# Kernel optimization log

Hardware: AMD Instinct MI355X
Metric: run time of the kernel (lower is better)

## Reference

```python
import jax, jax.numpy as jnp
import numpy as np

D_MODEL = 1024
D_FF = 4096          # shared expert hidden
NUM_M = 2
E_ROUTER = 8 * NUM_M - 1   # 15 router experts
D_FF_R = D_FF // NUM_M     # 2048 router expert hidden
TOP_K = NUM_M * 2 - 1      # 3
B, T = 2, 2048


def setup_inputs() -> dict:
    key = jax.random.key(0)
    ks = jax.random.split(key, 12)
    s = lambda fan_in: 1.0 / np.sqrt(fan_in)
    x = jax.random.normal(ks[0], (B, T, D_MODEL), dtype=jnp.float32)
    # shared experts stacked [S=1, ...]
    sW1 = jax.random.uniform(ks[1], (1, D_MODEL, D_FF), jnp.float32, -s(D_MODEL), s(D_MODEL))
    sb1 = jax.random.uniform(ks[2], (1, D_FF), jnp.float32, -s(D_MODEL), s(D_MODEL))
    sW2 = jax.random.uniform(ks[3], (1, D_FF, D_MODEL), jnp.float32, -s(D_FF), s(D_FF))
    sb2 = jax.random.uniform(ks[4], (1, D_MODEL), jnp.float32, -s(D_FF), s(D_FF))
    # router experts stacked [E, ...]
    rW1 = jax.random.uniform(ks[5], (E_ROUTER, D_MODEL, D_FF_R), jnp.float32, -s(D_MODEL), s(D_MODEL))
    rb1 = jax.random.uniform(ks[6], (E_ROUTER, D_FF_R), jnp.float32, -s(D_MODEL), s(D_MODEL))
    rW2 = jax.random.uniform(ks[7], (E_ROUTER, D_FF_R, D_MODEL), jnp.float32, -s(D_FF_R), s(D_FF_R))
    rb2 = jax.random.uniform(ks[8], (E_ROUTER, D_MODEL), jnp.float32, -s(D_FF_R), s(D_FF_R))
    # gating linear d_model -> E
    gW = jax.random.uniform(ks[9], (D_MODEL, E_ROUTER), jnp.float32, -s(D_MODEL), s(D_MODEL))
    gb = jax.random.uniform(ks[10], (E_ROUTER,), jnp.float32, -s(D_MODEL), s(D_MODEL))
    return {"x": x, "sW1": sW1, "sb1": sb1, "sW2": sW2, "sb2": sb2,
            "rW1": rW1, "rb1": rb1, "rW2": rW2, "rb2": rb2, "gW": gW, "gb": gb}


def _expert_stack(x, W1, b1, W2, b2):
    # x: [b,t,d]; W1: [e,d,f] -> out [e,b,t,d]
    h = jax.nn.gelu(jnp.einsum('btd,edf->ebtf', x, W1) + b1[:, None, None, :],
                    approximate=False)
    return jnp.einsum('ebtf,efd->ebtd', h, W2) + b2[:, None, None, :]


def reference(x, sW1, sb1, sW2, sb2, rW1, rb1, rW2, rb2, gW, gb):
    # shared experts (sum over S)
    shared_enc = _expert_stack(x, sW1, sb1, sW2, sb2).sum(0)  # [b,t,d]
    # gating: softmax then keep top-k values (no renormalization)
    weights = jax.nn.softmax(x @ gW + gb, axis=-1)            # [b,t,E]
    topv, topi = jax.lax.top_k(weights, TOP_K)                # [b,t,K]
    gated = (jax.nn.one_hot(topi, E_ROUTER, dtype=weights.dtype)
             * topv[..., None]).sum(axis=-2)                  # [b,t,E]
    # dense per-expert compute masked by sparse gates (faithful to source)
    router_out = _expert_stack(x, rW1, rb1, rW2, rb2)         # [E,b,t,d]
    router_enc = jnp.einsum('ebtd,bte->btd', router_out, gated)
    return shared_enc + router_enc + x
```

## Files before the change

kernel.cpp:

```cpp
#include <hip/hip_runtime.h>
#include <hip/hip_bf16.h>
#include <cstdint>
#include <cstddef>

#define TOKENS 4096
#define DM     1024
#define DFF    4096
#define NE     15
#define DFR    2048
#define NEX    17
#define MAXT   176

typedef float f32x4 __attribute__((ext_vector_type(4)));
typedef int   i32x4 __attribute__((ext_vector_type(4)));

__device__ __forceinline__ void mfma_16x16x32_bf16(f32x4& d, i32x4 a, i32x4 b){
  asm("v_mfma_f32_16x16x32_bf16 %0, %1, %2, %0" : "+v"(d) : "v"(a), "v"(b));
}

__device__ __forceinline__ void gload16(const void* g, void* l){
  __builtin_amdgcn_global_load_lds(
      (const __attribute__((address_space(1))) uint32_t*)g,
      (__attribute__((address_space(3))) uint32_t*)l, 16, 0, 0);
}

__device__ __forceinline__ unsigned short f2bf(float f){
  unsigned u = __float_as_uint(f);
  u += 0x7FFFu + ((u >> 16) & 1u);
  return (unsigned short)(u >> 16);
}

__device__ __forceinline__ float gelu_exact(float v){
  return 0.5f * v * (1.0f + erff(v * 0.70710678118654752440f));
}


__global__ void cast_x_kernel(const float* __restrict__ x, ushort* __restrict__ xb, int n4){
  int i = blockIdx.x*256 + threadIdx.x;
  if (i >= n4) return;
  float4 v = reinterpret_cast<const float4*>(x)[i];
  ushort4 o; o.x=f2bf(v.x); o.y=f2bf(v.y); o.z=f2bf(v.z); o.w=f2bf(v.w);
  reinterpret_cast<ushort4*>(xb)[i] = o;
}

__global__ void tcast_kernel(const float* __restrict__ src, ushort* __restrict__ dst, int R, int C){
  __shared__ float tile[32][33];
  const size_t bo = (size_t)blockIdx.z * R * C;
  const int c0 = blockIdx.x*32, r0 = blockIdx.y*32;
  const int tx = threadIdx.x, ty = threadIdx.y;
  #pragma unroll
  for (int i=0;i<4;i++){
    int r = ty + i*8;
    tile[r][tx] = src[bo + (size_t)(r0+r)*C + c0 + tx];
  }
  __syncthreads();
  #pragma unroll
  for (int i=0;i<4;i++){
    int r = ty + i*8;
    dst[bo + (size_t)(c0+r)*R + r0 + tx] = f2bf(tile[tx][r]);
  }
}


__global__ void gate_kernel(const float* __restrict__ x, const float* __restrict__ gW,
                            const float* __restrict__ gb,
                            int* __restrict__ tokexp, float* __restrict__ tokp){
  const int wave = threadIdx.x >> 6, lane = threadIdx.x & 63;
  const int token = blockIdx.x*4 + wave;
  const float* xr = x + (size_t)token * DM;
  float a[NE];
  #pragma unroll
  for (int e=0;e<NE;e++) a[e] = 0.f;
  const int d0 = lane * 16;
  float xv[16];
  #pragma unroll
  for (int j=0;j<4;j++){
    float4 v = reinterpret_cast<const float4*>(xr + d0)[j];
    xv[j*4+0]=v.x; xv[j*4+1]=v.y; xv[j*4+2]=v.z; xv[j*4+3]=v.w;
  }
  for (int j=0;j<16;j++){
    const float* gr = gW + (size_t)(d0 + j) * NE;
    #pragma unroll
    for (int e=0;e<NE;e++) a[e] += xv[j]*gr[e];
  }
  #pragma unroll
  for (int e=0;e<NE;e++){
    for (int off=32; off; off>>=1) a[e] += __shfl_xor(a[e], off, 64);
  }
  if (lane == 0){
    float l[NE], p[NE];
    float m = -1e30f;
    for (int e=0;e<NE;e++){ l[e] = a[e] + gb[e]; m = fmaxf(m, l[e]); }
    float s = 0.f;
    for (int e=0;e<NE;e++){ p[e] = expf(l[e]-m); s += p[e]; }
    float inv = 1.f/s;
    unsigned used = 0;
    for (int k=0;k<3;k++){
      int best = -1; float bv = -1e30f;
      for (int e=0;e<NE;e++) if (!((used>>e)&1u) && l[e] > bv){ bv = l[e]; best = e; }
      used |= 1u<<best;
      tokexp[token*3 + k] = best;
      tokp[token*3 + k]   = p[best]*inv;
    }
  }
}


__global__ void assign_kernel(const int* __restrict__ tokexp, const float* __restrict__ tokp,
                              int* __restrict__ counts, int* __restrict__ bases,
                              int* __restrict__ tokidx, float* __restrict__ gatev,
                              int* __restrict__ tokslot,
                              int* __restrict__ tile_e, int* __restrict__ tile_by,
                              int* __restrict__ ntiles){
  __shared__ int lh[256][NE];
  const int tid = threadIdx.x;
  const int t0 = tid * 16;

  int le[48];
  #pragma unroll
  for (int e=0;e<NE;e++) lh[tid][e] = 0;
  #pragma unroll
  for (int j=0;j<48;j++){
    int e = tokexp[t0*3 + j];
    le[j] = e;
    lh[tid][e]++;
  }
  __syncthreads();
  if (tid < NE){
    int run = 0;
    for (int i=0;i<256;i++){
      int v = lh[i][tid];
      lh[i][tid] = run;
      run += v;
    }
    counts[tid] = run;
  }
  __syncthreads();
  if (tid == 0){
    int b = 0;
    int t = 0;
    for (int e=0;e<NE;e++){
      int c = counts[e];
      bases[e] = b; b += ((c+127)>>7)<<7;
      int nb = (c+127)>>7;
      for (int j=0;j<nb;j++){ tile_e[t]=e; tile_by[t]=j; t++; }
    }
    bases[NE] = b; bases[NE+1] = b + TOKENS;
    for (int e=NE;e<NEX;e++){
      for (int j=0;j<32;j++){ tile_e[t]=e; tile_by[t]=j; t++; }
    }
    ntiles[0] = t;
  }
  __syncthreads();
  #pragma unroll
  for (int j=0;j<48;j++){
    const int t = t0 + (j/3), k = j - (j/3)*3;
    const int e = le[j];
    const int slot = lh[tid][e]++;
    const int idx = e*TOKENS + slot;
    tokidx[idx] = t;
    gatev[idx]  = tokp[t*3 + k];
    tokslot[t*3 + k] = idx;
  }
}


__global__ __launch_bounds__(256,3) void gemm1_kernel(
    const ushort* __restrict__ xb, const ushort* __restrict__ rW1T,
    const ushort* __restrict__ sW1T, const float* __restrict__ rb1,
    const float* __restrict__ sb1, const int* __restrict__ counts,
    const int* __restrict__ bases, const int* __restrict__ tokidx,
    const int* __restrict__ tile_e, const int* __restrict__ tile_by,
    const int* __restrict__ ntiles, ushort* __restrict__ h)
{
  const int ty = blockIdx.y;
  if (ty >= ntiles[0]) return;
  const int e = tile_e[ty], by = tile_by[ty], bx = blockIdx.x;
  const int cnt = (e < NE) ? counts[e] : TOKENS;

  __shared__ __align__(16) ushort lA[128*64];
  __shared__ __align__(16) ushort lB[128*64];

  const int tid = threadIdx.x, wave = tid >> 6, lane = tid & 63;
  const int wr = wave >> 1, wc = wave & 1;

  const ushort* Bp = (e < NE) ? (rW1T + ((size_t)e*DFR + (size_t)bx*128)*DM)
                              : (sW1T + ((size_t)(e-NE)*DFR + (size_t)bx*128)*DM);

  const ushort* srcA[4];
  const ushort* srcB[4];
  unsigned ldso[4];
  #pragma unroll
  for (int i=0;i<4;i++){
    const int rt = i*32 + wave*8 + (lane>>3);
    const int gr = by*128 + rt;
    const int tok = (e < NE) ? tokidx[e*TOKENS + (gr < cnt ? gr : cnt-1)] : gr;
    srcA[i] = xb + (size_t)tok*DM + (lane&7)*8;
    srcB[i] = Bp + (size_t)rt*DM + (lane&7)*8;
    ldso[i] = (unsigned)(i*4096 + wave*1024 + lane*16);
  }

  f32x4 zv = {0.f,0.f,0.f,0.f};
  f32x4 acc[4][4];
  #pragma unroll
  for (int m=0;m<4;m++){
    #pragma unroll
    for (int n=0;n<4;n++){ acc[m][n] = zv; }
  }

  for (int k0=0; k0<DM; k0+=64){
    __syncthreads();
    #pragma unroll
    for (int i=0;i<4;i++){ gload16(srcA[i]+k0, (char*)lA + ldso[i]); }
    #pragma unroll
    for (int i=0;i<4;i++){ gload16(srcB[i]+k0, (char*)lB + ldso[i]); }
    __syncthreads();
    #pragma unroll
    for (int kk=0; kk<2; kk++){
      i32x4 af[4], bfr[4];
      #pragma unroll
      for (int m=0;m<4;m++){
        af[m] = *(const i32x4*)((const char*)lA + ((wr*64 + m*16 + (lane&15))*128 + kk*64 + (lane>>4)*16));
      }
      #pragma unroll
      for (int n=0;n<4;n++){
        bfr[n] = *(const i32x4*)((const char*)lB + ((wc*64 + n*16 + (lane&15))*128 + kk*64 + (lane>>4)*16));
      }
      #pragma unroll
      for (int m=0;m<4;m++){
        #pragma unroll
        for (int n=0;n<4;n++){ mfma_16x16x32_bf16(acc[m][n], af[m], bfr[n]); }
      }
    }
  }

  const int hb = bases[e];
  const float* b1p = (e < NE) ? (rb1 + e*DFR + bx*128) : (sb1 + (e-NE)*DFR + bx*128);
  #pragma unroll
  for (int m=0;m<4;m++){
    #pragma unroll
    for (int n=0;n<4;n++){
      const int c = wc*64 + n*16 + (lane & 15);
      const float bias = b1p[c];
      #pragma unroll
      for (int i=0;i<4;i++){
        const int r = wr*64 + m*16 + (lane>>4)*4 + i;
        float v = acc[m][n][i] + bias;
        h[(size_t)(hb + by*128 + r)*DFR + (size_t)bx*128 + c] = f2bf(gelu_exact(v));
      }
    }
  }
}


__global__ __launch_bounds__(256,3) void gemm2_kernel(
    const ushort* __restrict__ h, const ushort* __restrict__ rW2T,
    const ushort* __restrict__ sW2T, const float* __restrict__ rb2,
    const float* __restrict__ sb2, const int* __restrict__ counts,
    const int* __restrict__ bases,
    const int* __restrict__ tile_e, const int* __restrict__ tile_by,
    const int* __restrict__ ntiles, ushort* __restrict__ rout)
{
  const int ty = blockIdx.y;
  if (ty >= ntiles[0]) return;
  const int e = tile_e[ty], by = tile_by[ty], bx = blockIdx.x;

  __shared__ __align__(16) ushort lA[128*64];
  __shared__ __align__(16) ushort lB[128*64];

  const int tid = threadIdx.x, wave = tid >> 6, lane = tid & 63;
  const int wr = wave >> 1, wc = wave & 1;

  const int hb = bases[e];
  const ushort* Ab = h + (size_t)(hb + by*128)*DFR;
  const ushort* Bp; size_t ldb;
  if (e < NE){ Bp = rW2T + ((size_t)e*DM + (size_t)bx*128)*DFR; ldb = DFR; }
  else       { Bp = sW2T + (size_t)(bx*128)*DFF + (size_t)(e-NE)*DFR; ldb = DFF; }

  const ushort* srcA[4];
  const ushort* srcB[4];
  unsigned ldso[4];
  #pragma unroll
  for (int i=0;i<4;i++){
    const int rt = i*32 + wave*8 + (lane>>3);
    srcA[i] = Ab + (size_t)rt*DFR + (lane&7)*8;
    srcB[i] = Bp + (size_t)rt*ldb + (lane&7)*8;
    ldso[i] = (unsigned)(i*4096 + wave*1024 + lane*16);
  }

  f32x4 zv = {0.f,0.f,0.f,0.f};
  f32x4 acc[4][4];
  #pragma unroll
  for (int m=0;m<4;m++){
    #pragma unroll
    for (int n=0;n<4;n++){ acc[m][n] = zv; }
  }

  for (int k0=0; k0<DFR; k0+=64){
    __syncthreads();
    #pragma unroll
    for (int i=0;i<4;i++){ gload16(srcA[i]+k0, (char*)lA + ldso[i]); }
    #pragma unroll
    for (int i=0;i<4;i++){ gload16(srcB[i]+k0, (char*)lB + ldso[i]); }
    __syncthreads();
    #pragma unroll
    for (int kk=0; kk<2; kk++){
      i32x4 af[4], bfr[4];
      #pragma unroll
      for (int m=0;m<4;m++){
        af[m] = *(const i32x4*)((const char*)lA + ((wr*64 + m*16 + (lane&15))*128 + kk*64 + (lane>>4)*16));
      }
      #pragma unroll
      for (int n=0;n<4;n++){
        bfr[n] = *(const i32x4*)((const char*)lB + ((wc*64 + n*16 + (lane&15))*128 + kk*64 + (lane>>4)*16));
      }
      #pragma unroll
      for (int m=0;m<4;m++){
        #pragma unroll
        for (int n=0;n<4;n++){ mfma_16x16x32_bf16(acc[m][n], af[m], bfr[n]); }
      }
    }
  }

  #pragma unroll
  for (int m=0;m<4;m++){
    #pragma unroll
    for (int n=0;n<4;n++){
      const int c  = wc*64 + n*16 + (lane & 15);
      const int cg = bx*128 + c;
      const float bias = (e < NE) ? rb2[e*DM + cg] : ((e == NE) ? sb2[cg] : 0.f);
      #pragma unroll
      for (int i=0;i<4;i++){
        const int r = wr*64 + m*16 + (lane>>4)*4 + i;
        rout[(size_t)(hb + by*128 + r)*DM + cg] = f2bf(acc[m][n][i] + bias);
      }
    }
  }
}


__global__ void combine_kernel(const float* __restrict__ x, const ushort* __restrict__ rout,
                               const int* __restrict__ bases, const int* __restrict__ tokslot,
                               const float* __restrict__ gatev, float* __restrict__ out)
{
  const int wave = threadIdx.x >> 6, lane = threadIdx.x & 63;
  const int token = blockIdx.x*4 + wave;
  const int d0 = lane*16;

  float acc[16];
  #pragma unroll
  for (int j=0;j<4;j++){
    float4 v = reinterpret_cast<const float4*>(x + (size_t)token*DM + d0)[j];
    acc[j*4+0]=v.x; acc[j*4+1]=v.y; acc[j*4+2]=v.z; acc[j*4+3]=v.w;
  }

  int   rows[5];
  float gs[5];
  rows[0] = bases[NE]   + token; gs[0] = 1.f;
  rows[1] = bases[NE+1] + token; gs[1] = 1.f;
  #pragma unroll
  for (int k=0;k<3;k++){
    const int idx = tokslot[token*3 + k];
    const int e = idx >> 12, s = idx & (TOKENS-1);
    rows[2+k] = bases[e] + s;
    gs[2+k] = gatev[idx];
  }

  #pragma unroll
  for (int q=0;q<5;q++){
    const float g = gs[q];
    const ushort* rp = rout + (size_t)rows[q]*DM + d0;
    #pragma unroll
    for (int h=0;h<2;h++){
      i32x4 v = *reinterpret_cast<const i32x4*>(rp + h*8);
      #pragma unroll
      for (int j=0;j<4;j++){
        const unsigned u = (unsigned)v[j];
        acc[h*8 + j*2 + 0] += g * __uint_as_float(u << 16);
        acc[h*8 + j*2 + 1] += g * __uint_as_float(u & 0xFFFF0000u);
      }
    }
  }

  #pragma unroll
  for (int j=0;j<4;j++){
    float4 v; v.x=acc[j*4+0]; v.y=acc[j*4+1]; v.z=acc[j*4+2]; v.w=acc[j*4+3];
    reinterpret_cast<float4*>(out + (size_t)token*DM + d0)[j] = v;
  }
}


extern "C" void kernel_launch(void* const* d_in, const int* in_sizes, int n_in,
                              void* d_out, int out_size, void* d_ws, size_t ws_size,
                              hipStream_t stream)
{
  (void)in_sizes; (void)n_in; (void)out_size; (void)ws_size;
  const float* x   = (const float*)d_in[0];
  const float* sW1 = (const float*)d_in[1];
  const float* sb1 = (const float*)d_in[2];
  const float* sW2 = (const float*)d_in[3];
  const float* sb2 = (const float*)d_in[4];
  const float* rW1 = (const float*)d_in[5];
  const float* rb1 = (const float*)d_in[6];
  const float* rW2 = (const float*)d_in[7];
  const float* rb2 = (const float*)d_in[8];
  const float* gW  = (const float*)d_in[9];
  const float* gb  = (const float*)d_in[10];
  float* out = (float*)d_out;

  char* ws = (char*)d_ws;
  ushort* xb   = (ushort*)(ws + 0);
  ushort* sW1T = (ushort*)(ws + 8388608);
  ushort* sW2T = (ushort*)(ws + 16777216);
  ushort* rW1T = (ushort*)(ws + 25165824);
  ushort* rW2T = (ushort*)(ws + 88080384);
  ushort* hbuf = (ushort*)(ws + 150994944);
  ushort* rout = (ushort*)(ws + 25165824);
  int*   counts  = (int*)(ws + 243269632);
  int*   bases   = (int*)(ws + 243269760);
  int*   tokidx  = (int*)(ws + 243270144);
  float* gatev   = (float*)(ws + 243515904);
  int*   tokslot = (int*)(ws + 243761664);
  int*   tokexp  = (int*)(ws + 243810816);
  float* tokp    = (float*)(ws + 243859968);
  int*   tile_e  = (int*)(ws + 243909120);
  int*   tile_by = (int*)(ws + 243910144);
  int*   ntiles  = (int*)(ws + 243911168);

  cast_x_kernel<<<dim3(TOKENS*DM/4/256), dim3(256), 0, stream>>>(x, xb, TOKENS*DM/4);
  tcast_kernel<<<dim3(DFF/32, DM/32, 1),  dim3(32,8), 0, stream>>>(sW1, sW1T, DM, DFF);
  tcast_kernel<<<dim3(DM/32, DFF/32, 1),  dim3(32,8), 0, stream>>>(sW2, sW2T, DFF, DM);
  tcast_kernel<<<dim3(DFR/32, DM/32, NE), dim3(32,8), 0, stream>>>(rW1, rW1T, DM, DFR);
  tcast_kernel<<<dim3(DM/32, DFR/32, NE), dim3(32,8), 0, stream>>>(rW2, rW2T, DFR, DM);

  gate_kernel<<<dim3(TOKENS/4), dim3(256), 0, stream>>>(x, gW, gb, tokexp, tokp);
  assign_kernel<<<dim3(1), dim3(256), 0, stream>>>(tokexp, tokp, counts, bases,
                                                   tokidx, gatev, tokslot,
                                                   tile_e, tile_by, ntiles);

  gemm1_kernel<<<dim3(16,MAXT), dim3(256), 0, stream>>>(
      xb, rW1T, sW1T, rb1, sb1, counts, bases, tokidx, tile_e, tile_by, ntiles, hbuf);
  gemm2_kernel<<<dim3(8,MAXT), dim3(256), 0, stream>>>(
      hbuf, rW2T, sW2T, rb2, sb2, counts, bases, tile_e, tile_by, ntiles, rout);
  combine_kernel<<<dim3(TOKENS/4), dim3(256), 0, stream>>>(
      x, rout, bases, tokslot, gatev, out);
}
```

Before: 420.8 us.

## Use 256x256 double-buffered swizzled GEMM tiles with 512 threads for expert GEMMs

Both expert GEMMs move from 128x128 tiles with 256 threads and a single LDS buffer to 256x256 tiles with 512 threads, two LDS stages (128KB) and XOR-swizzled layouts. The next k-slice is prefetched while the current one is computed, and MFMA issue runs at raised priority. The aim is more data reuse per loaded byte, fewer global loads, and overlap of loads with compute. In exchange each block uses much more LDS and registers, so occupancy drops, and with fewer, larger tiles the grid may fill the CUs less evenly.

```diff
diff --git a/kernel.cpp b/kernel.cpp
--- a/kernel.cpp
+++ b/kernel.cpp
@@ -9,7 +9,7 @@
 #define NE     15
 #define DFR    2048
 #define NEX    17
-#define MAXT   176
+#define MAXT   104
 
 typedef float f32x4 __attribute__((ext_vector_type(4)));
 typedef int   i32x4 __attribute__((ext_vector_type(4)));
@@ -141,13 +141,14 @@
     int t = 0;
     for (int e=0;e<NE;e++){
       int c = counts[e];
-      bases[e] = b; b += ((c+127)>>7)<<7;
-      int nb = (c+127)>>7;
-      for (int j=0;j<nb;j++){ tile_e[t]=e; tile_by[t]=j; t++; }
+      int prows = ((c+127)>>7)<<7;
+      bases[e] = b; b += prows;
+      int nb = (prows + 255) >> 8;
+      for (int j=0;j<nb && t<MAXT;j++){ tile_e[t]=e; tile_by[t]=j; t++; }
     }
     bases[NE] = b; bases[NE+1] = b + TOKENS;
     for (int e=NE;e<NEX;e++){
-      for (int j=0;j<32;j++){ tile_e[t]=e; tile_by[t]=j; t++; }
+      for (int j=0;j<16 && t<MAXT;j++){ tile_e[t]=e; tile_by[t]=j; t++; }
     }
     ntiles[0] = t;
   }
@@ -165,7 +166,53 @@
 }
 
 
-__global__ __launch_bounds__(256,3) void gemm1_kernel(
+#define GEMM_COMPUTE(BASEB)                                                          \
+  {                                                                                  \
+    const char* gbase = (BASEB);                                                     \
+    _Pragma("unroll")                                                                \
+    for (int p=0; p<4; ++p){                                                         \
+      const int qr = p>>1, qc = p&1;                                                 \
+      i32x4 af[2][4], bf[2][2];                                                      \
+      _Pragma("unroll")                                                              \
+      for (int kk=0; kk<2; kk++){                                                    \
+        const unsigned cb = (unsigned)((kk*64 + ((lane>>4)<<4)) ^ sw);               \
+        _Pragma("unroll")                                                            \
+        for (int m=0;m<4;m++){                                                       \
+          const int row = wr*128 + qr*64 + m*16 + (lane&15);                         \
+          af[kk][m] = *(const i32x4*)(gbase + row*128 + cb);                         \
+        }                                                                            \
+        _Pragma("unroll")                                                            \
+        for (int n=0;n<2;n++){                                                       \
+          const int row = wc*64 + qc*32 + n*16 + (lane&15);                          \
+          bf[kk][n] = *(const i32x4*)(gbase + 32768 + row*128 + cb);                 \
+        }                                                                            \
+      }                                                                              \
+      __builtin_amdgcn_s_setprio(1);                                                 \
+      _Pragma("unroll")                                                              \
+      for (int m=0;m<4;m++){                                                         \
+        _Pragma("unroll")                                                            \
+        for (int n=0;n<2;n++){                                                       \
+          mfma_16x16x32_bf16(acc[qr*4+m][qc*2+n], af[0][m], bf[0][n]);               \
+          mfma_16x16x32_bf16(acc[qr*4+m][qc*2+n], af[1][m], bf[1][n]);               \
+        }                                                                            \
+      }                                                                              \
+      __builtin_amdgcn_s_setprio(0);                                                 \
+    }                                                                                \
+  }
+
+#define GEMM_STAGE(BUF, T)                                                           \
+  {                                                                                  \
+    char* dA = smem + (size_t)(BUF)*65536;                                           \
+    char* dB = dA + 32768;                                                           \
+    _Pragma("unroll")                                                                \
+    for (int i=0;i<4;i++){                                                           \
+      gload16(aSrc[i] + (size_t)(T)*128, dA + i*8192 + tid*16);                      \
+      gload16(bSrc[i] + (size_t)(T)*128, dB + i*8192 + tid*16);                      \
+    }                                                                                \
+  }
+
+
+__global__ __launch_bounds__(512,2) void gemm1_kernel(
     const ushort* __restrict__ xb, const ushort* __restrict__ rW1T,
     const ushort* __restrict__ sW1T, const float* __restrict__ rb1,
     const float* __restrict__ sb1, const int* __restrict__ counts,
@@ -177,84 +224,78 @@
   if (ty >= ntiles[0]) return;
   const int e = tile_e[ty], by = tile_by[ty], bx = blockIdx.x;
   const int cnt = (e < NE) ? counts[e] : TOKENS;
-
-  __shared__ __align__(16) ushort lA[128*64];
-  __shared__ __align__(16) ushort lB[128*64];
-
-  const int tid = threadIdx.x, wave = tid >> 6, lane = tid & 63;
-  const int wr = wave >> 1, wc = wave & 1;
-
-  const ushort* Bp = (e < NE) ? (rW1T + ((size_t)e*DFR + (size_t)bx*128)*DM)
-                              : (sW1T + ((size_t)(e-NE)*DFR + (size_t)bx*128)*DM);
-
-  const ushort* srcA[4];
-  const ushort* srcB[4];
-  unsigned ldso[4];
+  const int prows = (e < NE) ? (((cnt+127)>>7)<<7) : TOKENS;
+
+  __shared__ __align__(16) char smem[131072];
+
+  const int tid = threadIdx.x;
+  const int wave = tid >> 6, lane = tid & 63;
+  const int wr = wave >> 2, wc = wave & 3;
+  const unsigned sw = (unsigned)((lane & 7) << 4);
+
+  const char* Bpb = (e < NE) ? (const char*)rW1T + ((size_t)e*DFR)*2048
+                             : (const char*)sW1T + ((size_t)(e-NE)*DFR)*2048;
+
+  const unsigned scol = (unsigned)(((tid & 7) << 4) ^ (((tid >> 3) & 7) << 4));
+  const char* aSrc[4];
+  const char* bSrc[4];
   #pragma unroll
   for (int i=0;i<4;i++){
-    const int rt = i*32 + wave*8 + (lane>>3);
-    const int gr = by*128 + rt;
-    const int tok = (e < NE) ? tokidx[e*TOKENS + (gr < cnt ? gr : cnt-1)] : gr;
-    srcA[i] = xb + (size_t)tok*DM + (lane&7)*8;
-    srcB[i] = Bp + (size_t)rt*DM + (lane&7)*8;
-    ldso[i] = (unsigned)(i*4096 + wave*1024 + lane*16);
-  }
-
-  f32x4 zv = {0.f,0.f,0.f,0.f};
-  f32x4 acc[4][4];
-  #pragma unroll
-  for (int m=0;m<4;m++){
-    #pragma unroll
-    for (int n=0;n<4;n++){ acc[m][n] = zv; }
-  }
-
-  for (int k0=0; k0<DM; k0+=64){
-    __syncthreads();
-    #pragma unroll
-    for (int i=0;i<4;i++){ gload16(srcA[i]+k0, (char*)lA + ldso[i]); }
-    #pragma unroll
-    for (int i=0;i<4;i++){ gload16(srcB[i]+k0, (char*)lB + ldso[i]); }
-    __syncthreads();
-    #pragma unroll
-    for (int kk=0; kk<2; kk++){
-      i32x4 af[4], bfr[4];
-      #pragma unroll
-      for (int m=0;m<4;m++){
-        af[m] = *(const i32x4*)((const char*)lA + ((wr*64 + m*16 + (lane&15))*128 + kk*64 + (lane>>4)*16));
+    const int rl = i*64 + (tid >> 3);
+    const int gr = by*256 + rl;
+    int tok;
+    if (e < NE){ const int cr = gr < cnt ? gr : cnt-1; tok = tokidx[e*TOKENS + cr]; }
+    else       { tok = gr < TOKENS ? gr : TOKENS-1; }
+    aSrc[i] = (const char*)xb + (size_t)tok*2048 + scol;
+    bSrc[i] = Bpb + (size_t)(bx*256 + rl)*2048 + scol;
+  }
+
+  f32x4 acc[8][4];
+  #pragma unroll
+  for (int m=0;m<8;m++){
+    #pragma unroll
+    for (int n=0;n<4;n++){ acc[m][n] = (f32x4){0.f,0.f,0.f,0.f}; }
+  }
+
+  const int NK = DM/64;
+  GEMM_STAGE(0, 0);
+  asm volatile("s_waitcnt vmcnt(0)" ::: "memory");
+  __builtin_amdgcn_s_barrier();
+  #pragma unroll 2
+  for (int t=0; t<NK-1; ++t){
+    GEMM_STAGE((t+1)&1, t+1);
+    asm volatile("s_waitcnt vmcnt(8)" ::: "memory");
+    __builtin_amdgcn_s_barrier();
+    GEMM_COMPUTE(smem + (size_t)(t&1)*65536);
+    __builtin_amdgcn_s_barrier();
+  }
+  asm volatile("s_waitcnt vmcnt(0)" ::: "memory");
+  __builtin_amdgcn_s_barrier();
+  GEMM_COMPUTE(smem + (size_t)((NK-1)&1)*65536);
+
+  const int hb = bases[e];
+  const float* b1p = (e < NE) ? (rb1 + e*DFR + bx*256) : (sb1 + (e-NE)*DFR + bx*256);
+  #pragma unroll
+  for (int m=0;m<8;m++){
+    const int rt = wr*128 + m*16 + (lane>>4)*4;
+    #pragma unroll
+    for (int i=0;i<4;i++){
+      const int gr = by*256 + rt + i;
+      if (gr < prows){
+        #pragma unroll
+        for (int n=0;n<4;n++){
+          const int c = wc*64 + n*16 + (lane & 15);
+          float v = acc[m][n][i] + b1p[c];
+          h[(size_t)(hb + gr)*DFR + (size_t)bx*256 + c] = f2bf(gelu_exact(v));
+        }
       }
-      #pragma unroll
-      for (int n=0;n<4;n++){
-        bfr[n] = *(const i32x4*)((const char*)lB + ((wc*64 + n*16 + (lane&15))*128 + kk*64 + (lane>>4)*16));
-      }
-      #pragma unroll
-      for (int m=0;m<4;m++){
-        #pragma unroll
-        for (int n=0;n<4;n++){ mfma_16x16x32_bf16(acc[m][n], af[m], bfr[n]); }
-      }
-    }
-  }
-
-  const int hb = bases[e];
-  const float* b1p = (e < NE) ? (rb1 + e*DFR + bx*128) : (sb1 + (e-NE)*DFR + bx*128);
-  #pragma unroll
-  for (int m=0;m<4;m++){
-    #pragma unroll
-    for (int n=0;n<4;n++){
-      const int c = wc*64 + n*16 + (lane & 15);
-      const float bias = b1p[c];
-      #pragma unroll
-      for (int i=0;i<4;i++){
-        const int r = wr*64 + m*16 + (lane>>4)*4 + i;
-        float v = acc[m][n][i] + bias;
-        h[(size_t)(hb + by*128 + r)*DFR + (size_t)bx*128 + c] = f2bf(gelu_exact(v));
-      }
-    }
-  }
-}
-
-
-__global__ __launch_bounds__(256,3) void gemm2_kernel(
-    const ushort* __restrict__ h, const ushort* __restrict__ rW2T,
+    }
+  }
+}
+
+
+__global__ __launch_bounds__(512,2) void gemm2_kernel(
+    const ushort* __restrict__ hbuf, const ushort* __restrict__ rW2T,
     const ushort* __restrict__ sW2T, const float* __restrict__ rb2,
     const float* __restrict__ sb2, const int* __restrict__ counts,
     const int* __restrict__ bases,
@@ -264,75 +305,69 @@
   const int ty = blockIdx.y;
   if (ty >= ntiles[0]) return;
   const int e = tile_e[ty], by = tile_by[ty], bx = blockIdx.x;
-
-  __shared__ __align__(16) ushort lA[128*64];
-  __shared__ __align__(16) ushort lB[128*64];
-
-  const int tid = threadIdx.x, wave = tid >> 6, lane = tid & 63;
-  const int wr = wave >> 1, wc = wave & 1;
-
+  const int cnt = (e < NE) ? counts[e] : TOKENS;
+  const int prows = (e < NE) ? (((cnt+127)>>7)<<7) : TOKENS;
   const int hb = bases[e];
-  const ushort* Ab = h + (size_t)(hb + by*128)*DFR;
-  const ushort* Bp; size_t ldb;
-  if (e < NE){ Bp = rW2T + ((size_t)e*DM + (size_t)bx*128)*DFR; ldb = DFR; }
-  else       { Bp = sW2T + (size_t)(bx*128)*DFF + (size_t)(e-NE)*DFR; ldb = DFF; }
-
-  const ushort* srcA[4];
-  const ushort* srcB[4];
-  unsigned ldso[4];
+
+  __shared__ __align__(16) char smem[131072];
+
+  const int tid = threadIdx.x;
+  const int wave = tid >> 6, lane = tid & 63;
+  const int wr = wave >> 2, wc = wave & 3;
+  const unsigned sw = (unsigned)((lane & 7) << 4);
+
+  const unsigned scol = (unsigned)(((tid & 7) << 4) ^ (((tid >> 3) & 7) << 4));
+  const char* aSrc[4];
+  const char* bSrc[4];
   #pragma unroll
   for (int i=0;i<4;i++){
-    const int rt = i*32 + wave*8 + (lane>>3);
-    srcA[i] = Ab + (size_t)rt*DFR + (lane&7)*8;
-    srcB[i] = Bp + (size_t)rt*ldb + (lane&7)*8;
-    ldso[i] = (unsigned)(i*4096 + wave*1024 + lane*16);
-  }
-
-  f32x4 zv = {0.f,0.f,0.f,0.f};
-  f32x4 acc[4][4];
-  #pragma unroll
-  for (int m=0;m<4;m++){
-    #pragma unroll
-    for (int n=0;n<4;n++){ acc[m][n] = zv; }
-  }
-
-  for (int k0=0; k0<DFR; k0+=64){
-    __syncthreads();
-    #pragma unroll
-    for (int i=0;i<4;i++){ gload16(srcA[i]+k0, (char*)lA + ldso[i]); }
-    #pragma unroll
-    for (int i=0;i<4;i++){ gload16(srcB[i]+k0, (char*)lB + ldso[i]); }
-    __syncthreads();
-    #pragma unroll
-    for (int kk=0; kk<2; kk++){
-      i32x4 af[4], bfr[4];
-      #pragma unroll
-      for (int m=0;m<4;m++){
-        af[m] = *(const i32x4*)((const char*)lA + ((wr*64 + m*16 + (lane&15))*128 + kk*64 + (lane>>4)*16));
-      }
-      #pragma unroll
-      for (int n=0;n<4;n++){
-        bfr[n] = *(const i32x4*)((const char*)lB + ((wc*64 + n*16 + (lane&15))*128 + kk*64 + (lane>>4)*16));
-      }
-      #pragma unroll
-      for (int m=0;m<4;m++){
+    const int rl = i*64 + (tid >> 3);
+    int ar = by*256 + rl; if (ar >= prows) ar = prows-1;
+    aSrc[i] = (const char*)hbuf + (size_t)(hb + ar)*4096 + scol;
+    if (e < NE){
+      bSrc[i] = (const char*)rW2T + ((size_t)e*DM + bx*256 + rl)*4096 + scol;
+    } else {
+      bSrc[i] = (const char*)sW2T + (size_t)(bx*256 + rl)*8192 + (size_t)(e-NE)*4096 + scol;
+    }
+  }
+
+  f32x4 acc[8][4];
+  #pragma unroll
+  for (int m=0;m<8;m++){
+    #pragma unroll
+    for (int n=0;n<4;n++){ acc[m][n] = (f32x4){0.f,0.f,0.f,0.f}; }
+  }
+
+  const int NK = DFR/64;
+  GEMM_STAGE(0, 0);
+  asm volatile("s_waitcnt vmcnt(0)" ::: "memory");
+  __builtin_amdgcn_s_barrier();
+  #pragma unroll 2
+  for (int t=0; t<NK-1; ++t){
+    GEMM_STAGE((t+1)&1, t+1);
+    asm volatile("s_waitcnt vmcnt(8)" ::: "memory");
+    __builtin_amdgcn_s_barrier();
+    GEMM_COMPUTE(smem + (size_t)(t&1)*65536);
+    __builtin_amdgcn_s_barrier();
+  }
+  asm volatile("s_waitcnt vmcnt(0)" ::: "memory");
+  __builtin_amdgcn_s_barrier();
+  GEMM_COMPUTE(smem + (size_t)((NK-1)&1)*65536);
+
+  #pragma unroll
+  for (int m=0;m<8;m++){
+    const int rt = wr*128 + m*16 + (lane>>4)*4;
+    #pragma unroll
+    for (int i=0;i<4;i++){
+      const int gr = by*256 + rt + i;
+      if (gr < prows){
         #pragma unroll
-        for (int n=0;n<4;n++){ mfma_16x16x32_bf16(acc[m][n], af[m], bfr[n]); }
-      }
-    }
-  }
-
-  #pragma unroll
-  for (int m=0;m<4;m++){
-    #pragma unroll
-    for (int n=0;n<4;n++){
-      const int c  = wc*64 + n*16 + (lane & 15);
-      const int cg = bx*128 + c;
-      const float bias = (e < NE) ? rb2[e*DM + cg] : ((e == NE) ? sb2[cg] : 0.f);
-      #pragma unroll
-      for (int i=0;i<4;i++){
-        const int r = wr*64 + m*16 + (lane>>4)*4 + i;
-        rout[(size_t)(hb + by*128 + r)*DM + cg] = f2bf(acc[m][n][i] + bias);
+        for (int n=0;n<4;n++){
+          const int c  = wc*64 + n*16 + (lane & 15);
+          const int cg = bx*256 + c;
+          const float bias = (e < NE) ? rb2[e*DM + cg] : ((e == NE) ? sb2[cg] : 0.f);
+          rout[(size_t)(hb + gr)*DM + cg] = f2bf(acc[m][n][i] + bias);
+        }
       }
     }
   }
@@ -438,9 +473,9 @@
                                                    tokidx, gatev, tokslot,
                                                    tile_e, tile_by, ntiles);
 
-  gemm1_kernel<<<dim3(16,MAXT), dim3(256), 0, stream>>>(
+  gemm1_kernel<<<dim3(8,MAXT), dim3(512), 0, stream>>>(
       xb, rW1T, sW1T, rb1, sb1, counts, bases, tokidx, tile_e, tile_by, ntiles, hbuf);
-  gemm2_kernel<<<dim3(8,MAXT), dim3(256), 0, stream>>>(
+  gemm2_kernel<<<dim3(4,MAXT), dim3(512), 0, stream>>>(
       hbuf, rW2T, sW2T, rb2, sb2, counts, bases, tile_e, tile_by, ntiles, rout);
   combine_kernel<<<dim3(TOKENS/4), dim3(256), 0, stream>>>(
       x, rout, bases, tokslot, gatev, out);
```

Result: slower. 491.9 us (+16.9%).
